# Kernel optimization log

Measured on AMD Instinct MI355X. Metric: run time of the kernel, lower is better.

The kernel has to match this reference:

```python
import jax, jax.numpy as jnp
import numpy as np

B, C, H, W = 4, 128, 64, 64
CO = 128

def setup_inputs() -> dict:
    key = jax.random.key(0)
    ks = jax.random.split(key, 10)
    s = 1.0 / np.sqrt(C)
    return {
        "x":  jax.random.normal(ks[0], (B, C, H, W), dtype=jnp.float32),
        "Wq": jax.random.uniform(ks[1], (C, C), jnp.float32, -s, s),
        "bq": jax.random.uniform(ks[2], (C,), jnp.float32, -s, s),
        "Wk": jax.random.uniform(ks[3], (C, C), jnp.float32, -s, s),
        "bk": jax.random.uniform(ks[4], (C,), jnp.float32, -s, s),
        "Wv": jax.random.uniform(ks[5], (C, C), jnp.float32, -s, s),
        "bv": jax.random.uniform(ks[6], (C,), jnp.float32, -s, s),
        "gamma": jnp.ones((1,), dtype=jnp.float32),
        "Wo": jax.random.uniform(ks[7], (CO, C), jnp.float32, -s, s),
        "bo": jax.random.uniform(ks[8], (CO,), jnp.float32, -s, s),
    }

def reference(x, Wq, bq, Wk, bk, Wv, bv, gamma, Wo, bo):
    b, c, h, w = x.shape
    xf = x.reshape(b, c, h * w)                       # [B,C,N]
    # 1x1 convs == channel matmuls
    Q = jnp.einsum('oc,bcn->bon', Wq, xf) + bq[None, :, None]
    K = jnp.einsum('oc,bcn->bon', Wk, xf) + bk[None, :, None]
    V = jnp.einsum('oc,bcn->bon', Wv, xf) + bv[None, :, None]
    # attention[b,i,j] = softmax_j( sum_c Q[b,c,i] K[b,c,j] )  (unscaled)
    scores = jnp.einsum('bci,bcj->bij', Q, K)         # [B,N,N]
    attn = jax.nn.softmax(scores, axis=-1)
    # selfAtten[b,c,i] = sum_j V[b,c,j] attn[b,i,j]
    sa = jnp.einsum('bcj,bij->bci', V, attn)          # [B,C,N]
    sa = gamma[0] * sa + xf
    out = jnp.einsum('oc,bcn->bon', Wo, sa) + bo[None, :, None]
    return out.reshape(b, Wo.shape[0], h, w)
```

## Files before the change

### kernel.cpp

```cpp
#include <hip/hip_runtime.h>

#define BB 4
#define CC 128
#define NN 4096

typedef float f32x4 __attribute__((ext_vector_type(4)));
typedef __bf16 bf16x8 __attribute__((ext_vector_type(8)));

#define MFMA16(A, B, C) __builtin_amdgcn_mfma_f32_16x16x32_bf16((A), (B), (C), 0, 0, 0)

typedef __attribute__((address_space(3))) void lds_void;
typedef __attribute__((address_space(1))) void glob_void;
#define GLD16(g, l) __builtin_amdgcn_global_load_lds((const glob_void*)(g), (lds_void*)(l), 16, 0, 0)

__device__ __forceinline__ int fK(int r) { return (r & 3) | (((r >> 3) & 1) << 2); }

__global__ __launch_bounds__(256)
void pack_w(const float* __restrict__ Wq, const float* __restrict__ bq,
            const float* __restrict__ Wk, const float* __restrict__ bk,
            const float* __restrict__ Wv, const float* __restrict__ bv,
            const float* __restrict__ Wo, const float* __restrict__ bo,
            __bf16* __restrict__ Wpk, float* __restrict__ bpk)
{
    const int mat = blockIdx.x >> 3;
    const int p   = blockIdx.x & 7;
    const int tid = threadIdx.x;
    const int ks  = tid >> 6;
    const int lane = tid & 63;
    const int col = lane & 15;
    const int quad = lane >> 4;

    const float LOG2E = 1.44269504088896340736f;
    const float* W = (mat == 0) ? Wq : (mat == 1) ? Wk : (mat == 2) ? Wv : Wo;
    const float* bsrc = (mat == 0) ? bq : (mat == 1) ? bk : (mat == 2) ? bv : bo;
    const float scale = (mat == 0) ? LOG2E : 1.0f;

    const float* wr = W + (size_t)(p * 16 + col) * CC + ks * 32 + quad * 8;
    float4 f0 = *(const float4*)wr;
    float4 f1 = *(const float4*)(wr + 4);
    bf16x8 a;
    a[0]=(__bf16)(f0.x*scale); a[1]=(__bf16)(f0.y*scale);
    a[2]=(__bf16)(f0.z*scale); a[3]=(__bf16)(f0.w*scale);
    a[4]=(__bf16)(f1.x*scale); a[5]=(__bf16)(f1.y*scale);
    a[6]=(__bf16)(f1.z*scale); a[7]=(__bf16)(f1.w*scale);
    *(bf16x8*)&Wpk[(((size_t)(mat * 8 + p) * 4 + ks) * 64 + lane) * 8] = a;

    if (p == 0 && tid < 128) bpk[mat * 128 + tid] = bsrc[tid] * scale;
}

__global__ __launch_bounds__(512, 2)
void qkv_gemm(const float* __restrict__ x,
              const __bf16* __restrict__ Wpk, const float* __restrict__ bpk,
              __bf16* __restrict__ Qt, __bf16* __restrict__ Kt,
              __bf16* __restrict__ Vblk)
{
    const int b    = blockIdx.y;
    const int n0   = blockIdx.x * 32;
    const int tid  = threadIdx.x;
    const int lane = tid & 63;
    const int wv   = __builtin_amdgcn_readfirstlane(tid >> 6);
    const int col  = lane & 15;
    const int quad = lane >> 4;

    __shared__ __bf16 xs[32 * 144];
    __shared__ __bf16 vs[128 * 32];

    {
        const int n  = tid & 31;
        const int c0 = tid >> 5;
        const float* xb = x + ((size_t)b * CC) * NN + n0 + n;
#pragma unroll
        for (int i = 0; i < 4; i++) {
            int c = (c0 + i * 16) * 2;
            float v0 = xb[(size_t)c * NN];
            float v1 = xb[(size_t)(c + 1) * NN];
            union { __bf16 h[2]; unsigned u; } pk;
            pk.h[0] = (__bf16)v0; pk.h[1] = (__bf16)v1;
            *(unsigned*)&xs[n * 144 + c] = pk.u;
        }
    }
    __syncthreads();

    bf16x8 Bf[2][4];
#pragma unroll
    for (int ng = 0; ng < 2; ng++)
#pragma unroll
        for (int ks = 0; ks < 4; ks++)
            Bf[ng][ks] = *(const bf16x8*)&xs[(ng * 16 + col) * 144 + ks * 32 + quad * 8];

#pragma unroll 1
    for (int mat = 0; mat < 3; mat++) {
        const int pg = wv;
        const int o0 = pg * 16;

        bf16x8 Af[4];
#pragma unroll
        for (int ks = 0; ks < 4; ks++)
            Af[ks] = *(const bf16x8*)&Wpk[(((size_t)(mat * 8 + pg) * 4 + ks) * 64 + lane) * 8];

        f32x4 D[2];
#pragma unroll
        for (int ng = 0; ng < 2; ng++) D[ng] = (f32x4){0.f, 0.f, 0.f, 0.f};
#pragma unroll
        for (int ks = 0; ks < 4; ks++)
#pragma unroll
            for (int ng = 0; ng < 2; ng++)
                D[ng] = MFMA16(Af[ks], Bf[ng][ks], D[ng]);

        float4 bias = *(const float4*)(bpk + mat * 128 + o0 + quad * 4);

#pragma unroll
        for (int ng = 0; ng < 2; ng++) {
            const int n = ng * 16 + col;
            float v[4];
#pragma unroll
            for (int r = 0; r < 4; r++)
                v[r] = D[ng][r] + ((const float*)&bias)[r];
            if (mat == 0) {
                union { __bf16 h[4]; uint2 u; } pk;
                for (int r = 0; r < 4; r++) pk.h[r] = (__bf16)v[r];
                *(uint2*)&Qt[((size_t)b * NN + n0 + n) * CC + o0 + quad * 4] = pk.u;
            } else if (mat == 1) {
                const int rin = ((n0 & 32) + n) & 63;
                const int chunk = ((o0 + quad * 4) >> 3) ^ fK(rin);
                union { __bf16 h[4]; uint2 u; } pk;
                for (int r = 0; r < 4; r++) pk.h[r] = (__bf16)v[r];
                *(uint2*)&Kt[((size_t)b * NN + n0 + n) * CC + chunk * 8 + (quad & 1) * 4] = pk.u;
            } else {
#pragma unroll
                for (int r = 0; r < 4; r++)
                    vs[(o0 + quad * 4 + r) * 32 + n] = (__bf16)v[r];
            }
        }
    }
    __syncthreads();

    {
        __bf16* vd = Vblk + (((size_t)b * 64 + (n0 >> 6)) * CC) * 64;
        const int chbase = (n0 & 32) >> 3;
        int idx = tid;
        int c = idx >> 2, chl = idx & 3;
        bf16x8 v = *(const bf16x8*)&vs[c * 32 + chl * 8];
        *(bf16x8*)&vd[c * 64 + (((chbase + chl) ^ (c & 7)) * 8)] = v;
    }
}

__global__ __launch_bounds__(256, 2)
void flash_attn(const __bf16* __restrict__ Qt, const __bf16* __restrict__ Kt,
                const __bf16* __restrict__ Vblk,
                float* __restrict__ Opart, float* __restrict__ Lpart)
{
    const int blk = blockIdx.x;
    const int b   = blk & 3;
    const int jhi = (blk >> 2) & 1;
    const int rr  = blk >> 3;
    const int js  = jhi * 2 + (rr & 1);
    const int i0  = (rr >> 1) * 128;

    const int tid  = threadIdx.x;
    const int lane = tid & 63;
    const int iw   = __builtin_amdgcn_readfirstlane(tid >> 6);
    const int col  = lane & 15;
    const int quad = lane >> 4;

    __shared__ __align__(16) char smem[69632];

#pragma unroll
    for (int e = 0; e < 8; e++) {
        int k = e * 256 + tid;
        __bf16* Vh = (__bf16*)(smem + (k >> 10) * 34816 + 16384);
        Vh[8192 + (k & 1023)] = (__bf16)(((k & 1023) < 64) ? 1.0f : 0.0f);
    }

    const __bf16* Qb = Qt + (size_t)b * NN * CC;
    const char*   Ks = (const char*)(Kt + (size_t)b * NN * CC);
    const char*   Vs = (const char*)(Vblk + ((size_t)b * 64 * CC) * 64);

    const int ibase = i0 + iw * 32;

    bf16x8 qf[2][4];
#pragma unroll
    for (int ig = 0; ig < 2; ig++)
#pragma unroll
        for (int ks = 0; ks < 4; ks++)
            qf[ig][ks] = *(const bf16x8*)(Qb + (size_t)(ibase + ig * 16 + col) * CC
                                             + ks * 32 + quad * 8);

    const int perm = ((col & 12) << 1) | (col & 3);
    const int fR   = fK(perm);
    int kaddr[4][4];
    const int joff[4] = {0, 4, 32, 36};
#pragma unroll
    for (int jg = 0; jg < 4; jg++)
#pragma unroll
        for (int ks = 0; ks < 4; ks++)
            kaddr[jg][ks] = (perm + joff[jg]) * 256 + (((ks * 4 + quad) ^ fR) * 16);
    int vaddr[8][2], oaddr[2];
#pragma unroll
    for (int cg = 0; cg < 8; cg++)
#pragma unroll
        for (int t = 0; t < 2; t++)
            vaddr[cg][t] = 16384 + (cg * 16 + col) * 128 + (((t * 4 + quad) ^ (col & 7)) * 16);
#pragma unroll
    for (int t = 0; t < 2; t++)
        oaddr[t] = 16384 + (128 + col) * 128 + (t * 4 + quad) * 16;

    f32x4 O[2][8], lacc[2];
#pragma unroll
    for (int ig = 0; ig < 2; ig++) {
#pragma unroll
        for (int cg = 0; cg < 8; cg++) O[ig][cg] = (f32x4){0.f, 0.f, 0.f, 0.f};
        lacc[ig] = (f32x4){0.f, 0.f, 0.f, 0.f};
    }

    {
        const char* kg = Ks + (size_t)(js * 16) * 16384;
        const char* vg = Vs + (size_t)(js * 16) * 16384;
#pragma unroll
        for (int q = 0; q < 4; q++) {
            const int call = iw * 4 + q;
            GLD16(kg + call * 1024 + lane * 16, smem + call * 1024 + lane * 16);
            GLD16(vg + call * 1024 + lane * 16, smem + 16384 + call * 1024 + lane * 16);
        }
    }

#pragma unroll 1
    for (int t16 = 0; t16 < 16; t16++) {
        __syncthreads();

        char* Buf = smem + (t16 & 1) * 34816;

        if (t16 < 15) {
            const int jt = js * 16 + t16 + 1;
            const char* kg = Ks + (size_t)jt * 16384;
            const char* vg = Vs + (size_t)jt * 16384;
            char* kd = smem + ((t16 + 1) & 1) * 34816;
#pragma unroll
            for (int q = 0; q < 4; q++) {
                const int call = iw * 4 + q;
                GLD16(kg + call * 1024 + lane * 16, kd + call * 1024 + lane * 16);
                GLD16(vg + call * 1024 + lane * 16, kd + 16384 + call * 1024 + lane * 16);
            }
        }

        f32x4 S[2][4];
#pragma unroll
        for (int ig = 0; ig < 2; ig++)
#pragma unroll
            for (int jg = 0; jg < 4; jg++)
                S[ig][jg] = (f32x4){-32.f, -32.f, -32.f, -32.f};
#pragma unroll
        for (int ks = 0; ks < 4; ks++) {
            bf16x8 k0 = *(const bf16x8*)(Buf + kaddr[0][ks]);
            bf16x8 k1 = *(const bf16x8*)(Buf + kaddr[1][ks]);
            bf16x8 k2 = *(const bf16x8*)(Buf + kaddr[2][ks]);
            bf16x8 k3 = *(const bf16x8*)(Buf + kaddr[3][ks]);
            S[0][0] = MFMA16(k0, qf[0][ks], S[0][0]);
            S[1][0] = MFMA16(k0, qf[1][ks], S[1][0]);
            S[0][1] = MFMA16(k1, qf[0][ks], S[0][1]);
            S[1][1] = MFMA16(k1, qf[1][ks], S[1][1]);
            S[0][2] = MFMA16(k2, qf[0][ks], S[0][2]);
            S[1][2] = MFMA16(k2, qf[1][ks], S[1][2]);
            S[0][3] = MFMA16(k3, qf[0][ks], S[0][3]);
            S[1][3] = MFMA16(k3, qf[1][ks], S[1][3]);
        }

#pragma unroll
        for (int ig = 0; ig < 2; ig++)
#pragma unroll
            for (int jg = 0; jg < 4; jg++)
#pragma unroll
                for (int r = 0; r < 4; r++)
                    S[ig][jg][r] = __builtin_amdgcn_exp2f(S[ig][jg][r]);

#pragma unroll
        for (int t = 0; t < 2; t++) {
            bf16x8 pf0, pf1;
#pragma unroll
            for (int e = 0; e < 8; e++) {
                int jg = 2 * t + (e >> 2), r = e & 3;
                pf0[e] = (__bf16)S[0][jg][r];
                pf1[e] = (__bf16)S[1][jg][r];
            }
#pragma unroll
            for (int cg = 0; cg < 8; cg++) {
                bf16x8 vf = *(const bf16x8*)(Buf + vaddr[cg][t]);
                O[0][cg] = MFMA16(vf, pf0, O[0][cg]);
                O[1][cg] = MFMA16(vf, pf1, O[1][cg]);
            }
            bf16x8 of = *(const bf16x8*)(Buf + oaddr[t]);
            lacc[0] = MFMA16(of, pf0, lacc[0]);
            lacc[1] = MFMA16(of, pf1, lacc[1]);
        }
    }
    __syncthreads();

    float* Ol = (float*)smem;
    float* Ll = (float*)(smem + 67584);
#pragma unroll
    for (int ig = 0; ig < 2; ig++) {
#pragma unroll
        for (int cg = 0; cg < 8; cg++)
#pragma unroll
            for (int r = 0; r < 4; r++)
                Ol[(cg * 16 + quad * 4 + r) * 132 + iw * 32 + ig * 16 + col] = O[ig][cg][r];
        if (quad == 0) Ll[iw * 32 + ig * 16 + col] = lacc[ig][0];
    }
    __syncthreads();
    {
        float* Od = Opart + (((size_t)b * 4 + js) * CC) * NN + i0;
#pragma unroll
        for (int e = 0; e < 16; e++) {
            int k = e * 256 + tid;
            int c = k >> 5, i4 = (k & 31) * 4;
            float4 v = *(const float4*)(Ol + c * 132 + i4);
            *(float4*)(Od + (size_t)c * NN + i4) = v;
        }
        if (tid < 128)
            Lpart[((size_t)b * 4 + js) * NN + i0 + tid] = Ll[tid];
    }
}

__global__ __launch_bounds__(256, 2)
void proj_out(const float* __restrict__ Opart, const float* __restrict__ Lpart,
              const float* __restrict__ x,
              const __bf16* __restrict__ Wpk, const float* __restrict__ bpk,
              const float* __restrict__ gamma, float* __restrict__ out)
{
    const int b    = blockIdx.y;
    const int n0   = blockIdx.x * 32;
    const int tid  = threadIdx.x;
    const int lane = tid & 63;
    const int wv   = __builtin_amdgcn_readfirstlane(tid >> 6);
    const int col  = lane & 15;
    const int quad = lane >> 4;

    __shared__ __bf16 sas[32 * 144];
    __shared__ float  outs[128 * 34];

    const float g = gamma[0];

    {
        const int n  = tid & 31;
        const int c0 = tid >> 5;
        const size_t nb = (size_t)b * 4;
        float l = Lpart[(nb + 0) * NN + n0 + n] + Lpart[(nb + 1) * NN + n0 + n]
                + Lpart[(nb + 2) * NN + n0 + n] + Lpart[(nb + 3) * NN + n0 + n];
        const float gl = g / l;
        const float* xb = x + ((size_t)b * CC) * NN + n0 + n;
        const float* Ob = Opart + (nb * CC) * NN + n0 + n;
#pragma unroll
        for (int i = 0; i < 8; i++) {
            int c = (c0 + i * 8) * 2;
            float s0 = 0.f, s1 = 0.f;
#pragma unroll
            for (int jsp = 0; jsp < 4; jsp++) {
                s0 += Ob[((size_t)jsp * CC + c) * NN];
                s1 += Ob[((size_t)jsp * CC + c + 1) * NN];
            }
            float v0 = xb[(size_t)c * NN] + s0 * gl;
            float v1 = xb[(size_t)(c + 1) * NN] + s1 * gl;
            union { __bf16 h[2]; unsigned u; } pk;
            pk.h[0] = (__bf16)v0; pk.h[1] = (__bf16)v1;
            *(unsigned*)&sas[n * 144 + c] = pk.u;
        }
    }
    __syncthreads();

    bf16x8 Bf[2][4];
#pragma unroll
    for (int ng = 0; ng < 2; ng++)
#pragma unroll
        for (int ks = 0; ks < 4; ks++)
            Bf[ng][ks] = *(const bf16x8*)&sas[(ng * 16 + col) * 144 + ks * 32 + quad * 8];

#pragma unroll
    for (int p = 0; p < 2; p++) {
        const int pg = wv * 2 + p;
        const int o0 = pg * 16;
        bf16x8 Af[4];
#pragma unroll
        for (int ks = 0; ks < 4; ks++)
            Af[ks] = *(const bf16x8*)&Wpk[(((size_t)(3 * 8 + pg) * 4 + ks) * 64 + lane) * 8];

        f32x4 D[2];
#pragma unroll
        for (int ng = 0; ng < 2; ng++) D[ng] = (f32x4){0.f, 0.f, 0.f, 0.f};
#pragma unroll
        for (int ks = 0; ks < 4; ks++)
#pragma unroll
            for (int ng = 0; ng < 2; ng++)
                D[ng] = MFMA16(Af[ks], Bf[ng][ks], D[ng]);

        float4 bias = *(const float4*)(bpk + 3 * 128 + o0 + quad * 4);
#pragma unroll
        for (int ng = 0; ng < 2; ng++)
#pragma unroll
            for (int r = 0; r < 4; r++)
                outs[(o0 + quad * 4 + r) * 34 + ng * 16 + col]
                    = D[ng][r] + ((const float*)&bias)[r];
    }
    __syncthreads();

    {
        float* od = out + ((size_t)b * CC) * NN + n0;
#pragma unroll
        for (int e = 0; e < 16; e++) {
            int k = e * 256 + tid;
            int o = k >> 5, n = k & 31;
            od[(size_t)o * NN + n] = outs[o * 34 + n];
        }
    }
}

extern "C" void kernel_launch(void* const* d_in, const int* in_sizes, int n_in,
                              void* d_out, int out_size, void* d_ws, size_t ws_size,
                              hipStream_t stream)
{
    const float* x  = (const float*)d_in[0];
    const float* Wq = (const float*)d_in[1];
    const float* bq = (const float*)d_in[2];
    const float* Wk = (const float*)d_in[3];
    const float* bk = (const float*)d_in[4];
    const float* Wv = (const float*)d_in[5];
    const float* bv = (const float*)d_in[6];
    const float* gm = (const float*)d_in[7];
    const float* Wo = (const float*)d_in[8];
    const float* bo = (const float*)d_in[9];

    __bf16* Qt    = (__bf16*)d_ws;
    __bf16* Kt    = Qt + (size_t)BB * NN * CC;
    __bf16* Vblk  = Kt + (size_t)BB * NN * CC;
    float*  Opart = (float*)(Vblk + (size_t)BB * NN * CC);
    float*  Lpart = Opart + (size_t)16 * CC * NN;
    __bf16* Wpk   = (__bf16*)(Lpart + (size_t)16 * NN);
    float*  bpk   = (float*)(Wpk + 4 * 8 * 4 * 64 * 8);
    float*  out   = (float*)d_out;

    pack_w<<<32, 256, 0, stream>>>(Wq, bq, Wk, bk, Wv, bv, Wo, bo, Wpk, bpk);
    qkv_gemm<<<dim3(128, 4), 512, 0, stream>>>(x, Wpk, bpk, Qt, Kt, Vblk);
    flash_attn<<<512, 256, 0, stream>>>(Qt, Kt, Vblk, Opart, Lpart);
    proj_out<<<dim3(128, 4), 256, 0, stream>>>(Opart, Lpart, x, Wpk, bpk, gm, out);
}
```

Measured before the change: 130.1 us.

## Store flash partial outputs as bf16 tiles and compute row sums in registers

The flash kernel now writes its per-split partial O accumulators as bf16 in a tiled [b,js,itile,c,128] layout instead of fp32 over the full N stride, halving the partial-result traffic written by flash_attn and read back by proj_out. The softmax denominator is accumulated in fp32 registers with cross-lane shuffles, replacing the extra MFMA against a ones block in LDS. This shrinks shared memory and removes two MFMAs per step. The cost is extra bf16 rounding of partial sums before they are combined.

```diff
diff --git a/kernel.cpp b/kernel.cpp
--- a/kernel.cpp
+++ b/kernel.cpp
@@ -148,14 +148,15 @@
 __global__ __launch_bounds__(256, 2)
 void flash_attn(const __bf16* __restrict__ Qt, const __bf16* __restrict__ Kt,
                 const __bf16* __restrict__ Vblk,
-                float* __restrict__ Opart, float* __restrict__ Lpart)
+                __bf16* __restrict__ Opart, float* __restrict__ Lpart)
 {
     const int blk = blockIdx.x;
     const int b   = blk & 3;
     const int jhi = (blk >> 2) & 1;
     const int rr  = blk >> 3;
     const int js  = jhi * 2 + (rr & 1);
-    const int i0  = (rr >> 1) * 128;
+    const int it  = rr >> 1;
+    const int i0  = it * 128;
 
     const int tid  = threadIdx.x;
     const int lane = tid & 63;
@@ -163,14 +164,7 @@
     const int col  = lane & 15;
     const int quad = lane >> 4;
 
-    __shared__ __align__(16) char smem[69632];
-
-#pragma unroll
-    for (int e = 0; e < 8; e++) {
-        int k = e * 256 + tid;
-        __bf16* Vh = (__bf16*)(smem + (k >> 10) * 34816 + 16384);
-        Vh[8192 + (k & 1023)] = (__bf16)(((k & 1023) < 64) ? 1.0f : 0.0f);
-    }
+    __shared__ __align__(16) char smem[65536];
 
     const __bf16* Qb = Qt + (size_t)b * NN * CC;
     const char*   Ks = (const char*)(Kt + (size_t)b * NN * CC);
@@ -195,23 +189,19 @@
 #pragma unroll
         for (int ks = 0; ks < 4; ks++)
             kaddr[jg][ks] = (perm + joff[jg]) * 256 + (((ks * 4 + quad) ^ fR) * 16);
-    int vaddr[8][2], oaddr[2];
+    int vaddr[8][2];
 #pragma unroll
     for (int cg = 0; cg < 8; cg++)
 #pragma unroll
         for (int t = 0; t < 2; t++)
             vaddr[cg][t] = 16384 + (cg * 16 + col) * 128 + (((t * 4 + quad) ^ (col & 7)) * 16);
-#pragma unroll
-    for (int t = 0; t < 2; t++)
-        oaddr[t] = 16384 + (128 + col) * 128 + (t * 4 + quad) * 16;
-
-    f32x4 O[2][8], lacc[2];
-#pragma unroll
-    for (int ig = 0; ig < 2; ig++) {
+
+    f32x4 O[2][8];
+    float lrun[2] = {0.f, 0.f};
+#pragma unroll
+    for (int ig = 0; ig < 2; ig++)
 #pragma unroll
         for (int cg = 0; cg < 8; cg++) O[ig][cg] = (f32x4){0.f, 0.f, 0.f, 0.f};
-        lacc[ig] = (f32x4){0.f, 0.f, 0.f, 0.f};
-    }
 
     {
         const char* kg = Ks + (size_t)(js * 16) * 16384;
@@ -228,13 +218,13 @@
     for (int t16 = 0; t16 < 16; t16++) {
         __syncthreads();
 
-        char* Buf = smem + (t16 & 1) * 34816;
+        char* Buf = smem + (t16 & 1) * 32768;
 
         if (t16 < 15) {
             const int jt = js * 16 + t16 + 1;
             const char* kg = Ks + (size_t)jt * 16384;
             const char* vg = Vs + (size_t)jt * 16384;
-            char* kd = smem + ((t16 + 1) & 1) * 34816;
+            char* kd = smem + ((t16 + 1) & 1) * 32768;
 #pragma unroll
             for (int q = 0; q < 4; q++) {
                 const int call = iw * 4 + q;
@@ -265,13 +255,18 @@
             S[1][3] = MFMA16(k3, qf[1][ks], S[1][3]);
         }
 
-#pragma unroll
-        for (int ig = 0; ig < 2; ig++)
-#pragma unroll
-            for (int jg = 0; jg < 4; jg++)
-#pragma unroll
-                for (int r = 0; r < 4; r++)
-                    S[ig][jg][r] = __builtin_amdgcn_exp2f(S[ig][jg][r]);
+        float s0 = 0.f, s1 = 0.f;
+#pragma unroll
+        for (int jg = 0; jg < 4; jg++)
+#pragma unroll
+            for (int r = 0; r < 4; r++) {
+                float p0 = __builtin_amdgcn_exp2f(S[0][jg][r]);
+                float p1 = __builtin_amdgcn_exp2f(S[1][jg][r]);
+                S[0][jg][r] = p0; s0 += p0;
+                S[1][jg][r] = p1; s1 += p1;
+            }
+        lrun[0] += s0;
+        lrun[1] += s1;
 
 #pragma unroll
         for (int t = 0; t < 2; t++) {
@@ -288,41 +283,38 @@
                 O[0][cg] = MFMA16(vf, pf0, O[0][cg]);
                 O[1][cg] = MFMA16(vf, pf1, O[1][cg]);
             }
-            bf16x8 of = *(const bf16x8*)(Buf + oaddr[t]);
-            lacc[0] = MFMA16(of, pf0, lacc[0]);
-            lacc[1] = MFMA16(of, pf1, lacc[1]);
-        }
-    }
-    __syncthreads();
-
-    float* Ol = (float*)smem;
-    float* Ll = (float*)(smem + 67584);
+        }
+    }
+    __syncthreads();
+
+    __bf16* Ol = (__bf16*)smem;
 #pragma unroll
     for (int ig = 0; ig < 2; ig++) {
+        lrun[ig] += __shfl_xor(lrun[ig], 16);
+        lrun[ig] += __shfl_xor(lrun[ig], 32);
 #pragma unroll
         for (int cg = 0; cg < 8; cg++)
 #pragma unroll
             for (int r = 0; r < 4; r++)
-                Ol[(cg * 16 + quad * 4 + r) * 132 + iw * 32 + ig * 16 + col] = O[ig][cg][r];
-        if (quad == 0) Ll[iw * 32 + ig * 16 + col] = lacc[ig][0];
-    }
-    __syncthreads();
-    {
-        float* Od = Opart + (((size_t)b * 4 + js) * CC) * NN + i0;
-#pragma unroll
-        for (int e = 0; e < 16; e++) {
-            int k = e * 256 + tid;
-            int c = k >> 5, i4 = (k & 31) * 4;
-            float4 v = *(const float4*)(Ol + c * 132 + i4);
-            *(float4*)(Od + (size_t)c * NN + i4) = v;
-        }
-        if (tid < 128)
-            Lpart[((size_t)b * 4 + js) * NN + i0 + tid] = Ll[tid];
+                Ol[(cg * 16 + quad * 4 + r) * 136 + iw * 32 + ig * 16 + col]
+                    = (__bf16)O[ig][cg][r];
+        if (quad == 0)
+            Lpart[((size_t)b * 4 + js) * NN + i0 + iw * 32 + ig * 16 + col] = lrun[ig];
+    }
+    __syncthreads();
+    {
+        __bf16* Od = Opart + ((size_t)((b * 4 + js) * 32 + it) * CC) * 128;
+#pragma unroll
+        for (int e = 0; e < 8; e++) {
+            int u = e * 256 + tid;
+            int c = u >> 4, ch = u & 15;
+            *(uint4*)&Od[c * 128 + ch * 8] = *(const uint4*)&Ol[c * 136 + ch * 8];
+        }
     }
 }
 
 __global__ __launch_bounds__(256, 2)
-void proj_out(const float* __restrict__ Opart, const float* __restrict__ Lpart,
+void proj_out(const __bf16* __restrict__ Opart, const float* __restrict__ Lpart,
               const float* __restrict__ x,
               const __bf16* __restrict__ Wpk, const float* __restrict__ bpk,
               const float* __restrict__ gamma, float* __restrict__ out)
@@ -343,20 +335,24 @@
     {
         const int n  = tid & 31;
         const int c0 = tid >> 5;
-        const size_t nb = (size_t)b * 4;
-        float l = Lpart[(nb + 0) * NN + n0 + n] + Lpart[(nb + 1) * NN + n0 + n]
-                + Lpart[(nb + 2) * NN + n0 + n] + Lpart[(nb + 3) * NN + n0 + n];
+        const int it = n0 >> 7;
+        const int io = (n0 & 127) + n;
+        float l = 0.f;
+#pragma unroll
+        for (int jsp = 0; jsp < 4; jsp++)
+            l += Lpart[((size_t)b * 4 + jsp) * NN + n0 + n];
         const float gl = g / l;
         const float* xb = x + ((size_t)b * CC) * NN + n0 + n;
-        const float* Ob = Opart + (nb * CC) * NN + n0 + n;
+        const __bf16* Ob = Opart + ((size_t)(b * 4) * 32 + it) * CC * 128;
 #pragma unroll
         for (int i = 0; i < 8; i++) {
             int c = (c0 + i * 8) * 2;
             float s0 = 0.f, s1 = 0.f;
 #pragma unroll
             for (int jsp = 0; jsp < 4; jsp++) {
-                s0 += Ob[((size_t)jsp * CC + c) * NN];
-                s1 += Ob[((size_t)jsp * CC + c + 1) * NN];
+                const __bf16* p = Ob + (size_t)jsp * (32 * CC * 128) + c * 128 + io;
+                s0 += (float)p[0];
+                s1 += (float)p[128];
             }
             float v0 = xb[(size_t)c * NN] + s0 * gl;
             float v1 = xb[(size_t)(c + 1) * NN] + s1 * gl;
@@ -431,8 +427,8 @@
     __bf16* Qt    = (__bf16*)d_ws;
     __bf16* Kt    = Qt + (size_t)BB * NN * CC;
     __bf16* Vblk  = Kt + (size_t)BB * NN * CC;
-    float*  Opart = (float*)(Vblk + (size_t)BB * NN * CC);
-    float*  Lpart = Opart + (size_t)16 * CC * NN;
+    __bf16* Opart = Vblk + (size_t)BB * NN * CC;
+    float*  Lpart = (float*)(Opart + (size_t)16 * 32 * CC * 128);
     __bf16* Wpk   = (__bf16*)(Lpart + (size_t)16 * NN);
     float*  bpk   = (float*)(Wpk + 4 * 8 * 4 * 64 * 8);
     float*  out   = (float*)d_out;
```

Result: no change. 127.6 us (-1.9%).
